# Kernel optimization log

Hardware: AMD Instinct MI355X
Metric: run time of the kernel (lower is better)

The kernel has to match this reference:

```python
import jax, jax.numpy as jnp
import numpy as np

BS, T, E, H, CU = 8, 1024, 512, 8, 6
HD = E // H
W_SCALE = 0.05  # keep pre-softmax logits in a sane range


def setup_inputs() -> dict:
    key = jax.random.key(0)
    ks = jax.random.split(key, 9)
    return {
        "x": jax.random.normal(ks[0], (BS, T, E), jnp.float32),
        "u": jax.random.normal(ks[1], (BS, CU, T, T), jnp.float32),
        "umask": jnp.zeros((BS, T, T, 1), jnp.bool_),
        "wq": jax.random.normal(ks[2], (E, E), jnp.float32) * W_SCALE,
        "wk": jax.random.normal(ks[3], (E, E), jnp.float32) * W_SCALE,
        "wv": jax.random.normal(ks[4], (E, E), jnp.float32) * W_SCALE,
        "wo": jax.random.normal(ks[5], (E, E), jnp.float32) * W_SCALE,
        "bo": jnp.zeros((E,), jnp.float32),
        "wu": jax.random.normal(ks[6], (H, CU), jnp.float32) * W_SCALE,
        "bu": jnp.zeros((H,), jnp.float32),
    }


def reference(x, u, umask, wq, wk, wv, wo, bo, wu, bu):
    bs, t, e = x.shape
    h, hd = H, HD
    scaling = hd ** (-0.5)

    # linear projections (torch Linear: y = x @ W^T), split heads -> [b, h, t, hd]
    def proj(w):
        return jnp.einsum('bte,fe->btf', x, w).reshape(bs, t, h, hd).transpose(0, 2, 1, 3)

    Q, K, V = proj(wq), proj(wk), proj(wv)

    # NOTE: faithful to source, which DIVIDES by head_dim**-0.5
    scores = jnp.einsum('bhqd,bhkd->bhqk', Q, K) / scaling

    # 1x1 conv bias projection: [b, cu, t, t] -> [b, h, t, t]
    ubias = jnp.einsum('bcij,hc->bhij', u, wu) + bu[None, :, None, None]
    # umask: [b, t, t, 1] -> swap dims 1 and 3 -> [b, 1, t, t]
    mask_t = jnp.transpose(umask, (0, 3, 2, 1))
    ubias = jnp.where(mask_t, -jnp.inf, ubias)
    scores = scores + ubias

    attn = jax.nn.softmax(scores, axis=-1)
    # dropout p=0.0 -> identity
    ctx = jnp.einsum('bhqk,bhkd->bqhd', attn, V).reshape(bs, t, e)
    out = jnp.einsum('bte,fe->btf', ctx, wo) + bo
    return (out, attn)
```

## Files before the change

### kernel.cpp

```cpp
#include <hip/hip_runtime.h>
#include <cmath>

#define BSZ 8
#define TT  1024
#define EE  512
#define HH  8
#define CUc 6
#define HDD 64

typedef __bf16 bf16;
typedef __attribute__((ext_vector_type(4))) float f32x4;
typedef __attribute__((ext_vector_type(8))) float f32x8;
typedef __attribute__((ext_vector_type(8))) bf16  bf16x8;

static __device__ __forceinline__ f32x4 mfma16(bf16x8 a, bf16x8 b, f32x4 c) {
    return __builtin_amdgcn_mfma_f32_16x16x32_bf16(a, b, c, 0, 0, 0);
}

__global__ __launch_bounds__(256) void k_split(const float* __restrict__ src,
                                               bf16* __restrict__ hi, bf16* __restrict__ lo, int n)
{
    const int i = (blockIdx.x * 256 + threadIdx.x) * 8;
    if (i >= n) return;
    f32x8 v = *(const f32x8*)(src + i);
    bf16x8 h8, l8;
#pragma unroll
    for (int k = 0; k < 8; ++k) {
        bf16 h = (bf16)v[k];
        h8[k] = h;
        l8[k] = (bf16)(v[k] - (float)h);
    }
    *(bf16x8*)(hi + i) = h8;
    if (lo) *(bf16x8*)(lo + i) = l8;
}

__global__ __launch_bounds__(256) void k_proj2(
    const float* __restrict__ x,
    const bf16* __restrict__ wqh, const bf16* __restrict__ wql,
    const bf16* __restrict__ wkh, const bf16* __restrict__ wkl,
    const bf16* __restrict__ wvh,
    bf16* __restrict__ Qh, bf16* __restrict__ Ql,
    bf16* __restrict__ Kh, bf16* __restrict__ Kl,
    bf16* __restrict__ Vt)
{
    const int rb = blockIdx.x;
    const int cb = blockIdx.y;
    const int wid = threadIdx.x >> 6;
    const int l   = threadIdx.x & 63;
    const int lg = l >> 4, lr = l & 15;
    const int row = rb * 64 + wid * 16 + lr;

    f32x4 aq[4], ak[4], av[4];
#pragma unroll
    for (int c = 0; c < 4; ++c) {
        aq[c] = f32x4{0.f,0.f,0.f,0.f}; ak[c] = f32x4{0.f,0.f,0.f,0.f}; av[c] = f32x4{0.f,0.f,0.f,0.f};
    }

    for (int ks = 0; ks < 16; ++ks) {
        const int e0 = ks * 32 + lg * 8;
        f32x8 xv = *(const f32x8*)(x + (size_t)row * EE + e0);
        bf16x8 xh, xl;
#pragma unroll
        for (int i = 0; i < 8; ++i) {
            bf16 h = (bf16)xv[i];
            xh[i] = h;
            xl[i] = (bf16)(xv[i] - (float)h);
        }
#pragma unroll
        for (int c = 0; c < 4; ++c) {
            const int f = cb * 64 + c * 16 + lr;
            const size_t wo = (size_t)f * EE + e0;
            bf16x8 qh = *(const bf16x8*)(wqh + wo);
            bf16x8 ql = *(const bf16x8*)(wql + wo);
            bf16x8 kh = *(const bf16x8*)(wkh + wo);
            bf16x8 kl = *(const bf16x8*)(wkl + wo);
            bf16x8 vh = *(const bf16x8*)(wvh + wo);
            aq[c] = mfma16(xh, qh, aq[c]); aq[c] = mfma16(xh, ql, aq[c]); aq[c] = mfma16(xl, qh, aq[c]);
            ak[c] = mfma16(xh, kh, ak[c]); ak[c] = mfma16(xh, kl, ak[c]); ak[c] = mfma16(xl, kh, ak[c]);
            av[c] = mfma16(xh, vh, av[c]);
        }
    }

#pragma unroll
    for (int c = 0; c < 4; ++c)
#pragma unroll
        for (int r = 0; r < 4; ++r) {
            const int orow = rb * 64 + wid * 16 + lg * 4 + r;
            const int b = orow >> 10, t = orow & 1023;
            const int f = cb * 64 + c * 16 + lr;
            const int h = f >> 6, d = f & 63;
            const size_t idx = ((size_t)(b * HH + h) * TT + t) * HDD + d;
            float vq = aq[c][r];
            bf16 qhi = (bf16)vq; Qh[idx] = qhi; Ql[idx] = (bf16)(vq - (float)qhi);
            float vk = ak[c][r];
            bf16 khi = (bf16)vk; Kh[idx] = khi; Kl[idx] = (bf16)(vk - (float)khi);
            Vt[(((size_t)(b * HH + h) * HDD + d) * TT) + t] = (bf16)av[c][r];
        }
}

__global__ __launch_bounds__(256) void k_ubias2(
    const float* __restrict__ u, const unsigned char* __restrict__ umask,
    const float* __restrict__ wu, const float* __restrict__ bu,
    float* __restrict__ A)
{
    __shared__ __align__(16) unsigned char msk[64][64];
    const int b  = blockIdx.z;
    const int i0 = blockIdx.y * 64;
    const int j0 = blockIdx.x * 64;
    const int t  = threadIdx.x;

    {
        const int jj  = t >> 2;
        const int seg = (t & 3) * 16;
        *(uint4*)(&msk[jj][seg]) =
            *(const uint4*)(umask + ((size_t)b * TT + (j0 + jj)) * TT + i0 + seg);
    }
    float wuv[HH][CUc], buv[HH];
#pragma unroll
    for (int h = 0; h < HH; ++h) {
        buv[h] = bu[h];
#pragma unroll
        for (int c = 0; c < CUc; ++c) wuv[h][c] = wu[h * CUc + c];
    }
    __syncthreads();

    const int j = j0 + (t & 63);
    for (int ii = (t >> 6); ii < 64; ii += 4) {
        const int i = i0 + ii;
        float uv[CUc];
#pragma unroll
        for (int c = 0; c < CUc; ++c)
            uv[c] = u[(((size_t)b * CUc + c) * TT + i) * TT + j];
        const bool mk = msk[t & 63][ii] != 0;
#pragma unroll
        for (int h = 0; h < HH; ++h) {
            float v = buv[h];
#pragma unroll
            for (int c = 0; c < CUc; ++c) v += uv[c] * wuv[h][c];
            if (mk) v = -INFINITY;
            bf16* ub = (bf16*)(A + ((size_t)(b * HH + h) * TT + (i & ~15)) * TT);
            ub[(i & 15) * TT + j] = (bf16)v;
        }
    }
}

__global__ __launch_bounds__(512, 2) void k_fused2(
    const bf16* __restrict__ Qh, const bf16* __restrict__ Ql,
    const bf16* __restrict__ Kh, const bf16* __restrict__ Kl,
    const bf16* __restrict__ Vt,
    float* __restrict__ A, bf16* __restrict__ ctx)
{
    const int bh = blockIdx.x & 63;
    const int ib = blockIdx.x >> 6;
    const int b  = bh >> 3, h = bh & 7;
    const int i0 = ib * 16;
    const int w  = threadIdx.x >> 6;
    const int l  = threadIdx.x & 63;
    const int lg = l >> 4, lr = l & 15;
    const int jw = w * 128;

    __shared__ __align__(16) bf16  P[16][1032];
    __shared__ __align__(16) float ctxred[8][16][64];
    __shared__ float mred[8][16], sred[8][16];

    const bf16* ubc = (const bf16*)(A + ((size_t)bh * TT + i0) * TT);
    bf16 ubv[8][4];
#pragma unroll
    for (int jt = 0; jt < 8; ++jt)
#pragma unroll
        for (int r = 0; r < 4; ++r)
            ubv[jt][r] = ubc[(size_t)(lg * 4 + r) * TT + jw + jt * 16 + lr];

    const bf16* qph = Qh + ((size_t)bh * TT + i0) * HDD;
    const bf16* qpl = Ql + ((size_t)bh * TT + i0) * HDD;
    bf16x8 qh0 = *(const bf16x8*)(qph + lr * HDD + lg * 8);
    bf16x8 qh1 = *(const bf16x8*)(qph + lr * HDD + 32 + lg * 8);
    bf16x8 ql0 = *(const bf16x8*)(qpl + lr * HDD + lg * 8);
    bf16x8 ql1 = *(const bf16x8*)(qpl + lr * HDD + 32 + lg * 8);

    const bf16* kph = Kh + (size_t)bh * TT * HDD;
    const bf16* kpl = Kl + (size_t)bh * TT * HDD;

    f32x4 s[8];
#pragma unroll
    for (int jt = 0; jt < 8; ++jt) {
        const int j = jw + jt * 16;
        bf16x8 kh0 = *(const bf16x8*)(kph + (size_t)(j + lr) * HDD + lg * 8);
        bf16x8 kh1 = *(const bf16x8*)(kph + (size_t)(j + lr) * HDD + 32 + lg * 8);
        bf16x8 kl0 = *(const bf16x8*)(kpl + (size_t)(j + lr) * HDD + lg * 8);
        bf16x8 kl1 = *(const bf16x8*)(kpl + (size_t)(j + lr) * HDD + 32 + lg * 8);
        f32x4 acc = f32x4{0.f,0.f,0.f,0.f};
        acc = mfma16(qh0, kh0, acc); acc = mfma16(qh1, kh1, acc);
        acc = mfma16(qh0, kl0, acc); acc = mfma16(qh1, kl1, acc);
        acc = mfma16(ql0, kh0, acc); acc = mfma16(ql1, kh1, acc);
#pragma unroll
        for (int r = 0; r < 4; ++r)
            acc[r] = acc[r] * 8.0f + (float)ubv[jt][r];
        s[jt] = acc;
    }

    float m[4];
#pragma unroll
    for (int r = 0; r < 4; ++r) {
        float mm = s[0][r];
#pragma unroll
        for (int jt = 1; jt < 8; ++jt) mm = fmaxf(mm, s[jt][r]);
        m[r] = mm;
    }
#pragma unroll
    for (int off = 1; off < 16; off <<= 1)
#pragma unroll
        for (int r = 0; r < 4; ++r) m[r] = fmaxf(m[r], __shfl_xor(m[r], off));

    float mexp[4];
#pragma unroll
    for (int r = 0; r < 4; ++r) mexp[r] = (m[r] == -INFINITY) ? 0.f : m[r];
    float sum[4] = {0.f, 0.f, 0.f, 0.f};
#pragma unroll
    for (int jt = 0; jt < 8; ++jt)
#pragma unroll
        for (int r = 0; r < 4; ++r) {
            float p = __expf(s[jt][r] - mexp[r]);
            s[jt][r] = p;
            sum[r] += p;
            P[lg * 4 + r][jw + jt * 16 + lr] = (bf16)p;
        }
#pragma unroll
    for (int off = 1; off < 16; off <<= 1)
#pragma unroll
        for (int r = 0; r < 4; ++r) sum[r] += __shfl_xor(sum[r], off);
    if (lr == 0)
#pragma unroll
        for (int r = 0; r < 4; ++r) { mred[w][lg * 4 + r] = m[r]; sred[w][lg * 4 + r] = sum[r]; }

    const bf16* vp = Vt + (size_t)bh * HDD * TT;
    f32x4 cacc[4];
#pragma unroll
    for (int dt = 0; dt < 4; ++dt) cacc[dt] = f32x4{0.f,0.f,0.f,0.f};
#pragma unroll
    for (int ks = 0; ks < 4; ++ks) {
        const int k0 = jw + ks * 32;
        bf16x8 a = *(const bf16x8*)(&P[lr][k0 + lg * 8]);
#pragma unroll
        for (int dt = 0; dt < 4; ++dt) {
            bf16x8 bv = *(const bf16x8*)(vp + (size_t)(dt * 16 + lr) * TT + k0 + lg * 8);
            cacc[dt] = mfma16(a, bv, cacc[dt]);
        }
    }
#pragma unroll
    for (int dt = 0; dt < 4; ++dt)
#pragma unroll
        for (int r = 0; r < 4; ++r)
            ctxred[w][lg * 4 + r][dt * 16 + lr] = cacc[dt][r];

    __syncthreads();

    float fac[4];
#pragma unroll
    for (int r = 0; r < 4; ++r) {
        const int row = lg * 4 + r;
        float M = mred[0][row];
#pragma unroll
        for (int wv = 1; wv < 8; ++wv) M = fmaxf(M, mred[wv][row]);
        float S = 0.f;
#pragma unroll
        for (int wv = 0; wv < 8; ++wv) S += sred[wv][row] * __expf(mred[wv][row] - M);
        fac[r] = __expf(m[r] - M) / S;
    }
    float* Ar = A + ((size_t)bh * TT + i0) * TT;
#pragma unroll
    for (int jt = 0; jt < 8; ++jt)
#pragma unroll
        for (int r = 0; r < 4; ++r)
            Ar[(size_t)(lg * 4 + r) * TT + jw + jt * 16 + lr] = s[jt][r] * fac[r];

    for (int o = threadIdx.x; o < 16 * 64; o += 512) {
        const int row = o >> 6, d = o & 63;
        float M = mred[0][row];
#pragma unroll
        for (int wv = 1; wv < 8; ++wv) M = fmaxf(M, mred[wv][row]);
        float S = 0.f, sm = 0.f;
#pragma unroll
        for (int wv = 0; wv < 8; ++wv) {
            const float e = __expf(mred[wv][row] - M);
            S  += sred[wv][row] * e;
            sm += ctxred[wv][row][d] * e;
        }
        ctx[((size_t)b * TT + i0 + row) * EE + h * HDD + d] = (bf16)(sm / S);
    }
}

__global__ __launch_bounds__(256) void k_out2(
    const bf16* __restrict__ ctx, const bf16* __restrict__ woh,
    const float* __restrict__ bo, float* __restrict__ out)
{
    const int rb = blockIdx.x;
    const int cb = blockIdx.y;
    const int wid = threadIdx.x >> 6;
    const int l = threadIdx.x & 63;
    const int lg = l >> 4, lr = l & 15;
    const int row = rb * 64 + wid * 16 + lr;

    f32x4 acc[4];
#pragma unroll
    for (int c = 0; c < 4; ++c) acc[c] = f32x4{0.f,0.f,0.f,0.f};

    for (int ks = 0; ks < 16; ++ks) {
        const int e0 = ks * 32 + lg * 8;
        bf16x8 af = *(const bf16x8*)(ctx + (size_t)row * EE + e0);
#pragma unroll
        for (int c = 0; c < 4; ++c) {
            const int f = cb * 64 + c * 16 + lr;
            bf16x8 wf = *(const bf16x8*)(woh + (size_t)f * EE + e0);
            acc[c] = mfma16(af, wf, acc[c]);
        }
    }
#pragma unroll
    for (int c = 0; c < 4; ++c) {
        const int f = cb * 64 + c * 16 + lr;
        const float bov = bo[f];
#pragma unroll
        for (int r = 0; r < 4; ++r) {
            const int orow = rb * 64 + wid * 16 + lg * 4 + r;
            out[(size_t)orow * EE + f] = acc[c][r] + bov;
        }
    }
}

extern "C" void kernel_launch(void* const* d_in, const int* in_sizes, int n_in,
                              void* d_out, int out_size, void* d_ws, size_t ws_size,
                              hipStream_t stream)
{
    (void)in_sizes; (void)n_in; (void)out_size; (void)ws_size;
    const float* x  = (const float*)d_in[0];
    const float* u  = (const float*)d_in[1];
    const unsigned char* umask = (const unsigned char*)d_in[2];
    const float* wq = (const float*)d_in[3];
    const float* wk = (const float*)d_in[4];
    const float* wv = (const float*)d_in[5];
    const float* wo = (const float*)d_in[6];
    const float* bo = (const float*)d_in[7];
    const float* wu = (const float*)d_in[8];
    const float* bu = (const float*)d_in[9];

    float* out = (float*)d_out;
    float* A   = out + (size_t)BSZ * TT * EE;

    const size_t qs = (size_t)BSZ * HH * TT * HDD;
    const size_t wsz = (size_t)EE * EE;
    bf16* Qh  = (bf16*)d_ws;
    bf16* Ql  = Qh + qs;
    bf16* Kh  = Ql + qs;
    bf16* Kl  = Kh + qs;
    bf16* Vt  = Kl + qs;
    bf16* ctx = Vt + qs;
    bf16* wqh = ctx + qs;
    bf16* wql = wqh + wsz;
    bf16* wkh = wql + wsz;
    bf16* wkl = wkh + wsz;
    bf16* wvh = wkl + wsz;
    bf16* woh = wvh + wsz;

    k_split<<<128, 256, 0, stream>>>(wq, wqh, wql, (int)wsz);
    k_split<<<128, 256, 0, stream>>>(wk, wkh, wkl, (int)wsz);
    k_split<<<128, 256, 0, stream>>>(wv, wvh, nullptr, (int)wsz);
    k_split<<<128, 256, 0, stream>>>(wo, woh, nullptr, (int)wsz);

    k_ubias2<<<dim3(16, 16, 8), 256, 0, stream>>>(u, umask, wu, bu, A);
    k_proj2 <<<dim3(128, 8), 256, 0, stream>>>(x, wqh, wql, wkh, wkl, wvh, Qh, Ql, Kh, Kl, Vt);
    k_fused2<<<4096, 512, 0, stream>>>(Qh, Ql, Kh, Kl, Vt, A, ctx);
    k_out2  <<<dim3(128, 8), 256, 0, stream>>>(ctx, woh, bo, out);
}
```

Before: 530.9 us.

## Merge split kernels, pre-split x, transpose ubias layout, raise fused occupancy

The four weight-split launches become one kernel, which also splits x into bf16 hi/lo once so that k_proj2 no longer re-splits x in every column block. The ubias staging buffer is stored transposed in 16-row chunks, so k_ubias3 writes bf16x8 vectors and k_fused3 reads bf16x4 vectors instead of scalar strided accesses. k_fused3 remaps block indices so blocks for the same batch share K/V, stores its cross-wave context reduction in bf16 to halve LDS use, and raises the launch-bounds occupancy hint from 2 to 6. The bf16 reduction buffer lowers accuracy, and the higher occupancy target may force register spills.

```diff
diff --git a/kernel.cpp b/kernel.cpp
--- a/kernel.cpp
+++ b/kernel.cpp
@@ -11,15 +11,30 @@
 typedef __bf16 bf16;
 typedef __attribute__((ext_vector_type(4))) float f32x4;
 typedef __attribute__((ext_vector_type(8))) float f32x8;
+typedef __attribute__((ext_vector_type(4))) bf16  bf16x4;
 typedef __attribute__((ext_vector_type(8))) bf16  bf16x8;
 
 static __device__ __forceinline__ f32x4 mfma16(bf16x8 a, bf16x8 b, f32x4 c) {
     return __builtin_amdgcn_mfma_f32_16x16x32_bf16(a, b, c, 0, 0, 0);
 }
 
-__global__ __launch_bounds__(256) void k_split(const float* __restrict__ src,
-                                               bf16* __restrict__ hi, bf16* __restrict__ lo, int n)
-{
+__global__ __launch_bounds__(256) void k_split_all(
+    const float* __restrict__ wq, const float* __restrict__ wk,
+    const float* __restrict__ wv, const float* __restrict__ wo,
+    const float* __restrict__ x,
+    bf16* __restrict__ wqh, bf16* __restrict__ wql,
+    bf16* __restrict__ wkh, bf16* __restrict__ wkl,
+    bf16* __restrict__ wvh, bf16* __restrict__ woh,
+    bf16* __restrict__ xh,  bf16* __restrict__ xl)
+{
+    const float* src; bf16* hi; bf16* lo; int n;
+    switch (blockIdx.y) {
+        case 0: src = wq; hi = wqh; lo = wql;     n = EE * EE;            break;
+        case 1: src = wk; hi = wkh; lo = wkl;     n = EE * EE;            break;
+        case 2: src = wv; hi = wvh; lo = nullptr; n = EE * EE;            break;
+        case 3: src = wo; hi = woh; lo = nullptr; n = EE * EE;            break;
+        default: src = x; hi = xh;  lo = xl;      n = BSZ * TT * EE;      break;
+    }
     const int i = (blockIdx.x * 256 + threadIdx.x) * 8;
     if (i >= n) return;
     f32x8 v = *(const f32x8*)(src + i);
@@ -35,7 +50,7 @@
 }
 
 __global__ __launch_bounds__(256) void k_proj2(
-    const float* __restrict__ x,
+    const bf16* __restrict__ xh, const bf16* __restrict__ xl,
     const bf16* __restrict__ wqh, const bf16* __restrict__ wql,
     const bf16* __restrict__ wkh, const bf16* __restrict__ wkl,
     const bf16* __restrict__ wvh,
@@ -58,14 +73,8 @@
 
     for (int ks = 0; ks < 16; ++ks) {
         const int e0 = ks * 32 + lg * 8;
-        f32x8 xv = *(const f32x8*)(x + (size_t)row * EE + e0);
-        bf16x8 xh, xl;
-#pragma unroll
-        for (int i = 0; i < 8; ++i) {
-            bf16 h = (bf16)xv[i];
-            xh[i] = h;
-            xl[i] = (bf16)(xv[i] - (float)h);
-        }
+        bf16x8 xhv = *(const bf16x8*)(xh + (size_t)row * EE + e0);
+        bf16x8 xlv = *(const bf16x8*)(xl + (size_t)row * EE + e0);
 #pragma unroll
         for (int c = 0; c < 4; ++c) {
             const int f = cb * 64 + c * 16 + lr;
@@ -75,9 +84,9 @@
             bf16x8 kh = *(const bf16x8*)(wkh + wo);
             bf16x8 kl = *(const bf16x8*)(wkl + wo);
             bf16x8 vh = *(const bf16x8*)(wvh + wo);
-            aq[c] = mfma16(xh, qh, aq[c]); aq[c] = mfma16(xh, ql, aq[c]); aq[c] = mfma16(xl, qh, aq[c]);
-            ak[c] = mfma16(xh, kh, ak[c]); ak[c] = mfma16(xh, kl, ak[c]); ak[c] = mfma16(xl, kh, ak[c]);
-            av[c] = mfma16(xh, vh, av[c]);
+            aq[c] = mfma16(xhv, qh, aq[c]); aq[c] = mfma16(xhv, ql, aq[c]); aq[c] = mfma16(xlv, qh, aq[c]);
+            ak[c] = mfma16(xhv, kh, ak[c]); ak[c] = mfma16(xhv, kl, ak[c]); ak[c] = mfma16(xlv, kh, ak[c]);
+            av[c] = mfma16(xhv, vh, av[c]);
         }
     }
 
@@ -98,7 +107,7 @@
         }
 }
 
-__global__ __launch_bounds__(256) void k_ubias2(
+__global__ __launch_bounds__(256) void k_ubias3(
     const float* __restrict__ u, const unsigned char* __restrict__ umask,
     const float* __restrict__ wu, const float* __restrict__ bu,
     float* __restrict__ A)
@@ -124,34 +133,48 @@
     }
     __syncthreads();
 
-    const int j = j0 + (t & 63);
-    for (int ii = (t >> 6); ii < 64; ii += 4) {
-        const int i = i0 + ii;
-        float uv[CUc];
-#pragma unroll
-        for (int c = 0; c < CUc; ++c)
-            uv[c] = u[(((size_t)b * CUc + c) * TT + i) * TT + j];
-        const bool mk = msk[t & 63][ii] != 0;
+    const int jl = t & 63;
+    const int j  = j0 + jl;
+    const int qi = t >> 6;
+    const int ibase = qi * 16;
+
+#pragma unroll
+    for (int g = 0; g < 2; ++g) {
+        bf16x8 o[HH];
+#pragma unroll
+        for (int ii2 = 0; ii2 < 8; ++ii2) {
+            const int ir = ibase + g * 8 + ii2;
+            const int i  = i0 + ir;
+            float uv[CUc];
+#pragma unroll
+            for (int c = 0; c < CUc; ++c)
+                uv[c] = u[(((size_t)b * CUc + c) * TT + i) * TT + j];
+            const bool mk = msk[jl][ir] != 0;
+#pragma unroll
+            for (int h = 0; h < HH; ++h) {
+                float v = buv[h];
+#pragma unroll
+                for (int c = 0; c < CUc; ++c) v += uv[c] * wuv[h][c];
+                o[h][ii2] = mk ? (bf16)(-INFINITY) : (bf16)v;
+            }
+        }
 #pragma unroll
         for (int h = 0; h < HH; ++h) {
-            float v = buv[h];
-#pragma unroll
-            for (int c = 0; c < CUc; ++c) v += uv[c] * wuv[h][c];
-            if (mk) v = -INFINITY;
-            bf16* ub = (bf16*)(A + ((size_t)(b * HH + h) * TT + (i & ~15)) * TT);
-            ub[(i & 15) * TT + j] = (bf16)v;
-        }
-    }
-}
-
-__global__ __launch_bounds__(512, 2) void k_fused2(
+            bf16* chunk = (bf16*)(A + ((size_t)(b * HH + h) * TT + i0 + ibase) * TT);
+            *(bf16x8*)(chunk + (size_t)j * 16 + g * 8) = o[h];
+        }
+    }
+}
+
+__global__ __launch_bounds__(512, 6) void k_fused3(
     const bf16* __restrict__ Qh, const bf16* __restrict__ Ql,
     const bf16* __restrict__ Kh, const bf16* __restrict__ Kl,
     const bf16* __restrict__ Vt,
     float* __restrict__ A, bf16* __restrict__ ctx)
 {
-    const int bh = blockIdx.x & 63;
-    const int ib = blockIdx.x >> 6;
+    const int g  = blockIdx.x;
+    const int bh = ((g >> 9) << 3) | (g & 7);
+    const int ib = (g >> 3) & 63;
     const int b  = bh >> 3, h = bh & 7;
     const int i0 = ib * 16;
     const int w  = threadIdx.x >> 6;
@@ -159,17 +182,15 @@
     const int lg = l >> 4, lr = l & 15;
     const int jw = w * 128;
 
-    __shared__ __align__(16) bf16  P[16][1032];
-    __shared__ __align__(16) float ctxred[8][16][64];
+    __shared__ __align__(16) bf16 P[16][1032];
+    __shared__ __align__(16) bf16 ctxred[8][16][64];
     __shared__ float mred[8][16], sred[8][16];
 
     const bf16* ubc = (const bf16*)(A + ((size_t)bh * TT + i0) * TT);
-    bf16 ubv[8][4];
+    bf16x4 ubv[8];
 #pragma unroll
     for (int jt = 0; jt < 8; ++jt)
-#pragma unroll
-        for (int r = 0; r < 4; ++r)
-            ubv[jt][r] = ubc[(size_t)(lg * 4 + r) * TT + jw + jt * 16 + lr];
+        ubv[jt] = *(const bf16x4*)(ubc + (size_t)(jw + jt * 16 + lr) * 16 + lg * 4);
 
     const bf16* qph = Qh + ((size_t)bh * TT + i0) * HDD;
     const bf16* qpl = Ql + ((size_t)bh * TT + i0) * HDD;
@@ -251,7 +272,7 @@
     for (int dt = 0; dt < 4; ++dt)
 #pragma unroll
         for (int r = 0; r < 4; ++r)
-            ctxred[w][lg * 4 + r][dt * 16 + lr] = cacc[dt][r];
+            ctxred[w][lg * 4 + r][dt * 16 + lr] = (bf16)cacc[dt][r];
 
     __syncthreads();
 
@@ -284,7 +305,7 @@
         for (int wv = 0; wv < 8; ++wv) {
             const float e = __expf(mred[wv][row] - M);
             S  += sred[wv][row] * e;
-            sm += ctxred[wv][row][d] * e;
+            sm += (float)ctxred[wv][row][d] * e;
         }
         ctx[((size_t)b * TT + i0 + row) * EE + h * HDD + d] = (bf16)(sm / S);
     }
@@ -346,8 +367,9 @@
     float* out = (float*)d_out;
     float* A   = out + (size_t)BSZ * TT * EE;
 
-    const size_t qs = (size_t)BSZ * HH * TT * HDD;
+    const size_t qs  = (size_t)BSZ * HH * TT * HDD;
     const size_t wsz = (size_t)EE * EE;
+    const size_t xs  = (size_t)BSZ * TT * EE;
     bf16* Qh  = (bf16*)d_ws;
     bf16* Ql  = Qh + qs;
     bf16* Kh  = Ql + qs;
@@ -360,14 +382,13 @@
     bf16* wkl = wkh + wsz;
     bf16* wvh = wkl + wsz;
     bf16* woh = wvh + wsz;
-
-    k_split<<<128, 256, 0, stream>>>(wq, wqh, wql, (int)wsz);
-    k_split<<<128, 256, 0, stream>>>(wk, wkh, wkl, (int)wsz);
-    k_split<<<128, 256, 0, stream>>>(wv, wvh, nullptr, (int)wsz);
-    k_split<<<128, 256, 0, stream>>>(wo, woh, nullptr, (int)wsz);
-
-    k_ubias2<<<dim3(16, 16, 8), 256, 0, stream>>>(u, umask, wu, bu, A);
-    k_proj2 <<<dim3(128, 8), 256, 0, stream>>>(x, wqh, wql, wkh, wkl, wvh, Qh, Ql, Kh, Kl, Vt);
-    k_fused2<<<4096, 512, 0, stream>>>(Qh, Ql, Kh, Kl, Vt, A, ctx);
+    bf16* xh  = woh + wsz;
+    bf16* xl  = xh  + xs;
+
+    k_split_all<<<dim3(2048, 5), 256, 0, stream>>>(wq, wk, wv, wo, x,
+                                                   wqh, wql, wkh, wkl, wvh, woh, xh, xl);
+    k_ubias3<<<dim3(16, 16, 8), 256, 0, stream>>>(u, umask, wu, bu, A);
+    k_proj2 <<<dim3(128, 8), 256, 0, stream>>>(xh, xl, wqh, wql, wkh, wkl, wvh, Qh, Ql, Kh, Kl, Vt);
+    k_fused3<<<4096, 512, 0, stream>>>(Qh, Ql, Kh, Kl, Vt, A, ctx);
     k_out2  <<<dim3(128, 8), 256, 0, stream>>>(ctx, woh, bo, out);
 }
```

Result: slower. 608.2 us (+14.5%).
